# Kernel optimization log

Hardware: AMD Instinct MI355X
Metric: run time of the kernel (lower is better)

The kernel has to match this reference:

```python
import jax, jax.numpy as jnp
import numpy as np

N_CLASSES = 80
N_ANCHORS = 3
IMAGE_SIZE = 608
STRIDE = 8
FSIZE = IMAGE_SIZE // STRIDE  # 76
BATCH = 16
N_BOX = 100
N_CH = 5 + N_CLASSES
IGNORE_THRE = 0.5
ANCHORS_PX = np.array([[13, 16], [28, 32], [62, 35]], dtype=np.float32)
MASKED_ANCHORS = ANCHORS_PX / IMAGE_SIZE / STRIDE  # grid-normalized anchors, [3,2]


def _bce(x, t):
    # torch F.binary_cross_entropy with log terms clamped at -100
    return -(t * jnp.maximum(jnp.log(x), -100.0)
             + (1.0 - t) * jnp.maximum(jnp.log(1.0 - x), -100.0))


def _iou_xyxy_ciou(a, b):
    # a: [N,4] xyxy, b: [M,4] xyxy -> CIoU [N,M] (standard YOLOv4 bboxes_iou, CIoU=True)
    tl = jnp.maximum(a[:, None, :2], b[None, :, :2])
    br = jnp.minimum(a[:, None, 2:], b[None, :, 2:])
    con_tl = jnp.minimum(a[:, None, :2], b[None, :, :2])
    con_br = jnp.maximum(a[:, None, 2:], b[None, :, 2:])
    area_a = jnp.prod(a[:, 2:] - a[:, :2], -1)
    area_b = jnp.prod(b[:, 2:] - b[:, :2], -1)
    en = jnp.all(tl < br, -1).astype(a.dtype)
    area_i = jnp.prod(br - tl, -1) * en
    iou = area_i / jnp.maximum(area_a[:, None] + area_b[None, :] - area_i, 1e-16)
    ctr_a = (a[:, :2] + a[:, 2:]) * 0.5
    ctr_b = (b[:, :2] + b[:, 2:]) * 0.5
    wh_a = a[:, 2:] - a[:, :2]
    wh_b = b[:, 2:] - b[:, :2]
    rho2 = jnp.sum((ctr_a[:, None] - ctr_b[None, :]) ** 2, -1)
    c2 = jnp.sum((con_br - con_tl) ** 2, -1)
    v = (4.0 / np.pi ** 2) * (jnp.arctan(wh_a[:, None, 0] / jnp.maximum(wh_a[:, None, 1], 1e-16))
                              - jnp.arctan(wh_b[None, :, 0] / jnp.maximum(wh_b[None, :, 1], 1e-16))) ** 2
    alpha = v / jnp.maximum(1.0 - iou + v, 1e-16)
    return iou - rho2 / jnp.maximum(c2, 1e-16) - alpha * v


def _iou_cxcywh(a, b):
    # a: [N,4] cx,cy,w,h ; b: [M,4] -> plain IoU [N,M]
    tl = jnp.maximum(a[:, None, :2] - a[:, None, 2:] * 0.5, b[None, :, :2] - b[None, :, 2:] * 0.5)
    br = jnp.minimum(a[:, None, :2] + a[:, None, 2:] * 0.5, b[None, :, :2] + b[None, :, 2:] * 0.5)
    area_a = jnp.prod(a[:, 2:], -1)
    area_b = jnp.prod(b[:, 2:], -1)
    en = jnp.all(tl < br, -1).astype(a.dtype)
    area_i = jnp.prod(br - tl, -1) * en
    return area_i / jnp.maximum(area_a[:, None] + area_b[None, :] - area_i, 1e-16)


def _prepare_one(pred_b, labels_b, masked_anchors, ref_anchors):
    # pred_b: [A,f,f,4] (cx,cy,w,h in grid units); labels_b: [N,5]
    n = labels_b.shape[0]
    lx = (labels_b[:, 0] + labels_b[:, 2]) / (STRIDE * 2)
    ly = (labels_b[:, 1] + labels_b[:, 3]) / (STRIDE * 2)
    lw = labels_b[:, 2] / STRIDE
    lh = labels_b[:, 3] / STRIDE
    li = lx.astype(jnp.int32)  # trunc toward zero (values positive)
    lj = ly.astype(jnp.int32)
    # anchor matching on (0,0,w,h) corner boxes vs ref anchors, CIoU
    box_wh = jnp.stack([jnp.zeros_like(lw), jnp.zeros_like(lh), lw, lh], -1)
    best_n_all = jnp.argmax(_iou_xyxy_ciou(box_wh, ref_anchors), axis=1)
    best_n = best_n_all % N_ANCHORS
    valid = best_n_all < N_ANCHORS  # anchor_masks == [0,1,2] -> always True here
    # ignore mask from pred IoU vs full label boxes
    label_box = jnp.stack([lx, ly, lw, lh], -1)
    pred_ious = _iou_cxcywh(pred_b.reshape(-1, 4), label_box)  # [A*f*f, N]
    obj = (~(jnp.max(pred_ious, axis=1) > IGNORE_THRE)).astype(jnp.float32)  # flat
    ncell = N_ANCHORS * FSIZE * FSIZE
    flat = jnp.where(valid, best_n * FSIZE * FSIZE + lj * FSIZE + li, ncell)  # OOB -> dropped
    obj = obj.at[flat].set(1.0, mode='drop')
    tmask = jnp.zeros((ncell, 4 + N_CLASSES), jnp.float32).at[flat].set(1.0, mode='drop')
    tx = lx - jnp.trunc(lx)
    aw = masked_anchors[best_n, 0]
    ah = masked_anchors[best_n, 1]
    rows = jnp.zeros((n, N_CH), jnp.float32)
    rows = rows.at[:, 0].set(tx).at[:, 1].set(tx)  # original uses label_x for both (kept faithful)
    rows = rows.at[:, 2].set(jnp.log(lw / aw + 1e-16))
    rows = rows.at[:, 3].set(jnp.log(lh / ah + 1e-16))
    rows = rows.at[:, 4].set(1.0)
    cls = labels_b[:, 4].astype(jnp.int32)
    rows = rows.at[jnp.arange(n), 5 + cls].set(1.0)
    target = jnp.zeros((ncell, N_CH), jnp.float32).at[flat].set(rows, mode='drop')
    scale_v = jnp.sqrt(2.0 - lw * lh / (FSIZE * FSIZE))
    tscale = jnp.zeros((ncell, 2), jnp.float32).at[flat].set(
        jnp.stack([scale_v, scale_v], -1), mode='drop')
    shp = (N_ANCHORS, FSIZE, FSIZE)
    return (obj.reshape(shp), tmask.reshape(shp + (4 + N_CLASSES,)),
            tscale.reshape(shp + (2,)), target.reshape(shp + (N_CH,)))


def _forward(x, labels):
    B = x.shape[0]
    out = x.reshape(B, N_ANCHORS, N_CH, FSIZE, FSIZE).transpose(0, 1, 3, 4, 2)
    sig = jax.nn.sigmoid(out)
    o01 = sig[..., :2]     # sigmoided xy
    o23r = out[..., 2:4]   # raw wh
    o4 = sig[..., 4]       # sigmoided obj
    ocls = sig[..., 5:]    # sigmoided cls
    grid = jnp.arange(FSIZE, dtype=x.dtype)
    masked_anchors = jnp.asarray(MASKED_ANCHORS)
    aw = masked_anchors[:, 0][None, :, None, None]
    ah = masked_anchors[:, 1][None, :, None, None]
    px = o01[..., 0] + grid[None, None, None, :]
    py = o01[..., 1] + grid[None, None, :, None]
    pw = jnp.exp(o23r[..., 0] * aw)  # faithful to original exp(raw * anchor)
    ph = jnp.exp(o23r[..., 1] * ah)
    pred_bbox = jnp.stack([px, py, pw, ph], -1)  # [B,3,f,f,4]
    ref_anchors = jnp.zeros((N_ANCHORS, 4), jnp.float32).at[:, 2:].set(masked_anchors)
    obj_mask, target_mask, target_scale, target = jax.vmap(
        _prepare_one, in_axes=(0, 0, None, None))(pred_bbox, labels, masked_anchors, ref_anchors)
    m01 = target_mask[..., :2]
    m23 = target_mask[..., 2:4]
    mcls = target_mask[..., 4:]
    o01m = o01 * m01
    o23m = o23r * m23 * target_scale
    o4m = o4 * obj_mask
    oclsm = ocls * mcls
    t01 = target[..., :2] * m01
    t23 = target[..., 2:4] * m23 * target_scale
    t4 = target[..., 4] * obj_mask
    tcls = target[..., 5:] * mcls
    w = target_scale * target_scale
    loss_xy = jnp.sum(w * _bce(o01m, t01))
    loss_wh = jnp.sum((o23m - t23) ** 2) / 2
    loss_obj = jnp.sum(_bce(o4m, t4))
    loss_cls = jnp.sum(_bce(oclsm, tcls))
    out_full = jnp.concatenate([o01m, o23m, o4m[..., None], oclsm], -1)
    tgt_full = jnp.concatenate([t01, t23, t4[..., None], tcls], -1)
    loss_l2 = jnp.sum((out_full - tgt_full) ** 2)
    loss = loss_xy + loss_wh + loss_obj + loss_cls
    return loss, loss_xy, loss_wh, loss_obj, loss_cls, loss_l2


def setup_inputs() -> dict:
    key = jax.random.key(0)
    k1, k2, k3, k4 = jax.random.split(key, 4)
    x = jax.random.normal(k1, (BATCH, N_ANCHORS * N_CH, FSIZE, FSIZE), jnp.float32)
    xy = jax.random.uniform(k2, (BATCH, N_BOX, 2), jnp.float32, 0.0, IMAGE_SIZE / 2)
    wh = jax.random.uniform(k3, (BATCH, N_BOX, 2), jnp.float32, float(STRIDE), IMAGE_SIZE / 2)
    cls = jax.random.randint(k4, (BATCH, N_BOX, 1), 0, N_CLASSES).astype(jnp.float32)
    labels = jnp.concatenate([xy, wh, cls], -1)  # [B, N_BOX, 5]
    return {"x": x, "labels": labels}


def reference(x, labels):
    return _forward(x, labels)
```

## Files before the change

kernel.cpp:

```cpp
#include <hip/hip_runtime.h>
#include <math.h>

#define FS      76
#define NCELLP  (FS*FS)
#define NA      3
#define NCH     85
#define NB      16
#define NLAB    100
#define NCLS    80
#define BLK     256
#define GX      ((NCELLP + BLK - 1) / BLK)
#define NBLK    (GX * NA * NB)

__device__ __forceinline__ float sigf(float z) { return 1.0f / (1.0f + expf(-z)); }

__device__ __forceinline__ float bcef(float x, float t) {
    return -(t * fmaxf(logf(x), -100.0f) + (1.0f - t) * fmaxf(logf(1.0f - x), -100.0f));
}

__global__ __launch_bounds__(BLK) void k_main(const float* __restrict__ x,
                                              const float* __restrict__ labels,
                                              double* __restrict__ part)
{
    const float AW[3] = {13.0f/4864.0f, 28.0f/4864.0f, 62.0f/4864.0f};
    const float AH[3] = {16.0f/4864.0f, 32.0f/4864.0f, 35.0f/4864.0f};

    __shared__ float4 s_box[NLAB];
    __shared__ float  s_area[NLAB];
    __shared__ int    s_flat[NLAB];
    __shared__ float  s_tx[NLAB], s_tw[NLAB], s_th[NLAB], s_sv[NLAB];
    __shared__ int    s_cls[NLAB];
    __shared__ int    s_win[BLK];
    __shared__ float4 s_cbox[NLAB];
    __shared__ float  s_carea[NLAB];
    __shared__ int    s_ncand, s_nw;
    __shared__ int    s_wlist[BLK];
    __shared__ float  s_pmax[BLK/64];
    __shared__ float  s_red[BLK/64][5];

    const int a = blockIdx.y, b = blockIdx.z;
    const int tid = threadIdx.x;

    s_win[tid] = -1;
    if (tid == 0) { s_ncand = 0; s_nw = 0; }
    if (tid < NLAB) {
        const float* L = labels + (size_t)(b * NLAB + tid) * 5;
        const float lx = (L[0] + L[2]) * 0.0625f;
        const float ly = (L[1] + L[3]) * 0.0625f;
        const float lw = L[2] * 0.125f;
        const float lh = L[3] * 0.125f;
        const int li = (int)lx, lj = (int)ly;

        const float area_a = lw * lh;
        const float ata = atanf(lw / fmaxf(lh, 1e-16f));
        const float V4PI2 = (float)(4.0 / (M_PI * M_PI));
        float best = -1e30f; int bn = 0;
        #pragma unroll
        for (int n = 0; n < NA; n++) {
            const float aw = AW[n], ah = AH[n];
            const float brx = fminf(lw, aw), bry = fminf(lh, ah);
            const float ai  = (0.0f < brx && 0.0f < bry) ? brx * bry : 0.0f;
            const float iou = ai / fmaxf(area_a + aw * ah - ai, 1e-16f);
            const float dx = (lw - aw) * 0.5f, dy = (lh - ah) * 0.5f;
            const float rho2 = dx * dx + dy * dy;
            const float cx = fmaxf(lw, aw), cy = fmaxf(lh, ah);
            const float c2 = cx * cx + cy * cy;
            const float da = ata - atanf(aw / fmaxf(ah, 1e-16f));
            const float v = V4PI2 * da * da;
            const float alpha = v / fmaxf(1.0f - iou + v, 1e-16f);
            const float ciou = iou - rho2 / fmaxf(c2, 1e-16f) - alpha * v;
            if (ciou > best) { best = ciou; bn = n; }
        }
        s_box[tid]  = make_float4(lx - lw * 0.5f, ly - lh * 0.5f,
                                  lx + lw * 0.5f, ly + lh * 0.5f);
        s_area[tid] = area_a;
        s_flat[tid] = bn * NCELLP + lj * FS + li;
        s_tx[tid]   = lx - truncf(lx);
        s_tw[tid]   = logf(lw / AW[bn] + 1e-16f);
        s_th[tid]   = logf(lh / AH[bn] + 1e-16f);
        s_sv[tid]   = sqrtf(2.0f - area_a / (float)NCELLP);
        s_cls[tid]  = (int)L[4];
    }
    __syncthreads();

    const int p = blockIdx.x * BLK + tid;
    const bool live = (p < NCELLP);
    const int pc = live ? p : (NCELLP - 1);
    const float* xb = x + ((size_t)(b * NA + a) * NCH) * NCELLP + pc;
    const float o0 = xb[0];
    const float o1 = xb[(size_t)1 * NCELLP];
    const float o2 = xb[(size_t)2 * NCELLP];
    const float o3 = xb[(size_t)3 * NCELLP];
    const float o4 = xb[(size_t)4 * NCELLP];
    const float s0 = sigf(o0), s1 = sigf(o1), s4 = sigf(o4);
    const float pw = expf(o2 * AW[a]), ph = expf(o3 * AH[a]);
    const float pa = live ? pw * ph : 0.0f;

    if (tid < NLAB) {
        const int idx = s_flat[tid] - (a * NCELLP + blockIdx.x * BLK);
        if (idx >= 0 && idx < BLK) atomicMax(&s_win[idx], tid);
    }
    float m = pa;
    #pragma unroll
    for (int off = 32; off > 0; off >>= 1) m = fmaxf(m, __shfl_xor(m, off, 64));
    if ((tid & 63) == 0) s_pmax[tid >> 6] = m;
    __syncthreads();
    const float pmax = fmaxf(fmaxf(s_pmax[0], s_pmax[1]), fmaxf(s_pmax[2], s_pmax[3]));

    if (tid < NLAB && s_area[tid] < 2.0f * pmax) {
        const int q = atomicAdd(&s_ncand, 1);
        s_cbox[q] = s_box[tid];
        s_carea[q] = s_area[tid];
    }
    __syncthreads();

    float axy = 0.f, awh = 0.f, aobj = 0.f, acls = 0.f, al2 = 0.f;
    int win = -1;
    if (live) {
        const int j = p / FS, i = p - j * FS;
        const float px = s0 + (float)i, py = s1 + (float)j;
        const float px1 = px - pw * 0.5f, px2 = px + pw * 0.5f;
        const float py1 = py - ph * 0.5f, py2 = py + ph * 0.5f;

        bool anyhit = false;
        const int nc = s_ncand;
        for (int l = 0; l < nc; l++) {
            const float4 bb = s_cbox[l];
            const float tlx = fmaxf(px1, bb.x);
            const float tly = fmaxf(py1, bb.y);
            const float brx = fminf(px2, bb.z);
            const float bry = fminf(py2, bb.w);
            const float ai = (tlx < brx && tly < bry) ? (brx - tlx) * (bry - tly) : 0.0f;
            anyhit = anyhit || (2.0f * ai > pa + s_carea[l] - ai);
        }
        win = s_win[tid];

        const float obj = (win >= 0) ? 1.0f : (anyhit ? 0.0f : 1.0f);
        if (obj != 0.0f) {
            const float t4 = (win >= 0) ? 1.0f : 0.0f;
            aobj += bcef(s4, t4);
            const float d4 = s4 - t4;
            al2 += d4 * d4;
        }
        if (win >= 0) {
            const float tx = s_tx[win], tw = s_tw[win], th = s_th[win], sv = s_sv[win];
            const float w2 = sv * sv;
            axy += w2 * (bcef(s0, tx) + bcef(s1, tx));
            const float dw = (o2 - tw) * sv, dh = (o3 - th) * sv;
            awh += dw * dw + dh * dh;
            const float d0 = s0 - tx, d1 = s1 - tx;
            al2 += d0 * d0 + d1 * d1 + dw * dw + dh * dh;
            const int q = atomicAdd(&s_nw, 1);
            s_wlist[q] = (tid << 16) | win;
        }
    }
    __syncthreads();

    const int nw = s_nw;
    for (int e = 0; e < nw; e++) {
        const int pk = s_wlist[e];
        const int wtid = pk >> 16, wl = pk & 0xffff;
        if (tid < NCLS) {
            const int cellp = blockIdx.x * BLK + wtid;
            const float sc = sigf(x[((size_t)(b * NA + a) * NCH + 5 + tid) * NCELLP + cellp]);
            const float t = (tid == s_cls[wl]) ? 1.0f : 0.0f;
            acls += bcef(sc, t);
            const float dc = sc - t;
            al2 += dc * dc;
        }
    }

    float v[5] = {axy, awh, aobj, acls, al2};
    #pragma unroll
    for (int k = 0; k < 5; k++) {
        float t = v[k];
        for (int off = 32; off > 0; off >>= 1) t += __shfl_down(t, off, 64);
        v[k] = t;
    }
    const int wave = tid >> 6, lane = tid & 63;
    if (lane == 0) {
        #pragma unroll
        for (int k = 0; k < 5; k++) s_red[wave][k] = v[k];
    }
    __syncthreads();
    if (tid == 0) {
        const int bid = blockIdx.x + GX * (blockIdx.y + NA * blockIdx.z);
        #pragma unroll
        for (int k = 0; k < 5; k++) {
            double s = 0.0;
            for (int w = 0; w < BLK/64; w++) s += (double)s_red[w][k];
            part[(size_t)bid * 5 + k] = s;
        }
    }
}

__global__ __launch_bounds__(256) void k_final(const double* __restrict__ part,
                                               float* __restrict__ out)
{
    __shared__ double s_red[4][5];
    const int tid = threadIdx.x;
    double v[5] = {0, 0, 0, 0, 0};
    for (int r = tid; r < NBLK; r += 256) {
        #pragma unroll
        for (int k = 0; k < 5; k++) v[k] += part[(size_t)r * 5 + k];
    }
    #pragma unroll
    for (int k = 0; k < 5; k++) {
        double t = v[k];
        for (int off = 32; off > 0; off >>= 1) t += __shfl_down(t, off, 64);
        v[k] = t;
    }
    const int wave = tid >> 6, lane = tid & 63;
    if (lane == 0) {
        #pragma unroll
        for (int k = 0; k < 5; k++) s_red[wave][k] = v[k];
    }
    __syncthreads();
    if (tid == 0) {
        double xy = 0, wh = 0, ob = 0, cl = 0, l2 = 0;
        for (int w = 0; w < 4; w++) {
            xy += s_red[w][0]; wh += s_red[w][1]; ob += s_red[w][2];
            cl += s_red[w][3]; l2 += s_red[w][4];
        }
        wh *= 0.5;
        out[0] = (float)(xy + wh + ob + cl);
        out[1] = (float)xy;
        out[2] = (float)wh;
        out[3] = (float)ob;
        out[4] = (float)cl;
        out[5] = (float)l2;
    }
}

extern "C" void kernel_launch(void* const* d_in, const int* in_sizes, int n_in,
                              void* d_out, int out_size, void* d_ws, size_t ws_size,
                              hipStream_t stream) {
    const float* x      = (const float*)d_in[0];
    const float* labels = (const float*)d_in[1];
    double* part = (double*)d_ws;

    dim3 grid(GX, NA, NB);
    k_main<<<grid, BLK, 0, stream>>>(x, labels, part);
    k_final<<<1, 256, 0, stream>>>(part, (float*)d_out);
}
```

Before: 132.4 us.

## Fuse final reduction via float atomics and hoist global loads before label setup

Drops the second reduction kernel: each block now adds its partial sums straight into the six outputs with float atomicAdd, after a memset of the output. The five channel loads from x are moved ahead of the label preprocessing so their latency overlaps the per-label CIoU and atan math. The per-wave pmax exchange is replaced by an integer atomicMax on the float bits, which is valid because the values are non-negative. The output now accumulates in float with a nondeterministic order instead of a double tree, and a memset is added to the launch sequence.

```diff
diff --git a/kernel.cpp b/kernel.cpp
--- a/kernel.cpp
+++ b/kernel.cpp
@@ -10,7 +10,6 @@
 #define NCLS    80
 #define BLK     256
 #define GX      ((NCELLP + BLK - 1) / BLK)
-#define NBLK    (GX * NA * NB)
 
 __device__ __forceinline__ float sigf(float z) { return 1.0f / (1.0f + expf(-z)); }
 
@@ -20,7 +19,7 @@
 
 __global__ __launch_bounds__(BLK) void k_main(const float* __restrict__ x,
                                               const float* __restrict__ labels,
-                                              double* __restrict__ part)
+                                              float* __restrict__ out)
 {
     const float AW[3] = {13.0f/4864.0f, 28.0f/4864.0f, 62.0f/4864.0f};
     const float AH[3] = {16.0f/4864.0f, 32.0f/4864.0f, 35.0f/4864.0f};
@@ -33,16 +32,25 @@
     __shared__ int    s_win[BLK];
     __shared__ float4 s_cbox[NLAB];
     __shared__ float  s_carea[NLAB];
-    __shared__ int    s_ncand, s_nw;
+    __shared__ int    s_ncand, s_nw, s_pmaxbits;
     __shared__ int    s_wlist[BLK];
-    __shared__ float  s_pmax[BLK/64];
     __shared__ float  s_red[BLK/64][5];
 
     const int a = blockIdx.y, b = blockIdx.z;
     const int tid = threadIdx.x;
 
+    const int p = blockIdx.x * BLK + tid;
+    const bool live = (p < NCELLP);
+    const int pc = live ? p : (NCELLP - 1);
+    const float* xb = x + ((size_t)(b * NA + a) * NCH) * NCELLP + pc;
+    const float o0 = xb[0];
+    const float o1 = xb[(size_t)1 * NCELLP];
+    const float o2 = xb[(size_t)2 * NCELLP];
+    const float o3 = xb[(size_t)3 * NCELLP];
+    const float o4 = xb[(size_t)4 * NCELLP];
+
     s_win[tid] = -1;
-    if (tid == 0) { s_ncand = 0; s_nw = 0; }
+    if (tid == 0) { s_ncand = 0; s_nw = 0; s_pmaxbits = 0; }
     if (tid < NLAB) {
         const float* L = labels + (size_t)(b * NLAB + tid) * 5;
         const float lx = (L[0] + L[2]) * 0.0625f;
@@ -83,15 +91,6 @@
     }
     __syncthreads();
 
-    const int p = blockIdx.x * BLK + tid;
-    const bool live = (p < NCELLP);
-    const int pc = live ? p : (NCELLP - 1);
-    const float* xb = x + ((size_t)(b * NA + a) * NCH) * NCELLP + pc;
-    const float o0 = xb[0];
-    const float o1 = xb[(size_t)1 * NCELLP];
-    const float o2 = xb[(size_t)2 * NCELLP];
-    const float o3 = xb[(size_t)3 * NCELLP];
-    const float o4 = xb[(size_t)4 * NCELLP];
     const float s0 = sigf(o0), s1 = sigf(o1), s4 = sigf(o4);
     const float pw = expf(o2 * AW[a]), ph = expf(o3 * AH[a]);
     const float pa = live ? pw * ph : 0.0f;
@@ -103,9 +102,9 @@
     float m = pa;
     #pragma unroll
     for (int off = 32; off > 0; off >>= 1) m = fmaxf(m, __shfl_xor(m, off, 64));
-    if ((tid & 63) == 0) s_pmax[tid >> 6] = m;
-    __syncthreads();
-    const float pmax = fmaxf(fmaxf(s_pmax[0], s_pmax[1]), fmaxf(s_pmax[2], s_pmax[3]));
+    if ((tid & 63) == 0) atomicMax(&s_pmaxbits, __float_as_int(m));
+    __syncthreads();
+    const float pmax = __int_as_float(s_pmaxbits);
 
     if (tid < NLAB && s_area[tid] < 2.0f * pmax) {
         const int q = atomicAdd(&s_ncand, 1);
@@ -115,7 +114,6 @@
     __syncthreads();
 
     float axy = 0.f, awh = 0.f, aobj = 0.f, acls = 0.f, al2 = 0.f;
-    int win = -1;
     if (live) {
         const int j = p / FS, i = p - j * FS;
         const float px = s0 + (float)i, py = s1 + (float)j;
@@ -133,7 +131,7 @@
             const float ai = (tlx < brx && tly < bry) ? (brx - tlx) * (bry - tly) : 0.0f;
             anyhit = anyhit || (2.0f * ai > pa + s_carea[l] - ai);
         }
-        win = s_win[tid];
+        const int win = s_win[tid];
 
         const float obj = (win >= 0) ? 1.0f : (anyhit ? 0.0f : 1.0f);
         if (obj != 0.0f) {
@@ -184,51 +182,22 @@
     }
     __syncthreads();
     if (tid == 0) {
-        const int bid = blockIdx.x + GX * (blockIdx.y + NA * blockIdx.z);
+        double s[5];
         #pragma unroll
         for (int k = 0; k < 5; k++) {
-            double s = 0.0;
-            for (int w = 0; w < BLK/64; w++) s += (double)s_red[w][k];
-            part[(size_t)bid * 5 + k] = s;
-        }
-    }
-}
-
-__global__ __launch_bounds__(256) void k_final(const double* __restrict__ part,
-                                               float* __restrict__ out)
-{
-    __shared__ double s_red[4][5];
-    const int tid = threadIdx.x;
-    double v[5] = {0, 0, 0, 0, 0};
-    for (int r = tid; r < NBLK; r += 256) {
-        #pragma unroll
-        for (int k = 0; k < 5; k++) v[k] += part[(size_t)r * 5 + k];
-    }
-    #pragma unroll
-    for (int k = 0; k < 5; k++) {
-        double t = v[k];
-        for (int off = 32; off > 0; off >>= 1) t += __shfl_down(t, off, 64);
-        v[k] = t;
-    }
-    const int wave = tid >> 6, lane = tid & 63;
-    if (lane == 0) {
-        #pragma unroll
-        for (int k = 0; k < 5; k++) s_red[wave][k] = v[k];
-    }
-    __syncthreads();
-    if (tid == 0) {
-        double xy = 0, wh = 0, ob = 0, cl = 0, l2 = 0;
-        for (int w = 0; w < 4; w++) {
-            xy += s_red[w][0]; wh += s_red[w][1]; ob += s_red[w][2];
-            cl += s_red[w][3]; l2 += s_red[w][4];
-        }
-        wh *= 0.5;
-        out[0] = (float)(xy + wh + ob + cl);
-        out[1] = (float)xy;
-        out[2] = (float)wh;
-        out[3] = (float)ob;
-        out[4] = (float)cl;
-        out[5] = (float)l2;
+            double t = 0.0;
+            for (int w = 0; w < BLK/64; w++) t += (double)s_red[w][k];
+            s[k] = t;
+        }
+        s[1] *= 0.5;
+        const float xy = (float)s[0], wh = (float)s[1], ob = (float)s[2],
+                    cl = (float)s[3], l2 = (float)s[4];
+        atomicAdd(&out[0], xy + wh + ob + cl);
+        atomicAdd(&out[1], xy);
+        atomicAdd(&out[2], wh);
+        atomicAdd(&out[3], ob);
+        atomicAdd(&out[4], cl);
+        atomicAdd(&out[5], l2);
     }
 }
 
@@ -237,9 +206,10 @@
                               hipStream_t stream) {
     const float* x      = (const float*)d_in[0];
     const float* labels = (const float*)d_in[1];
-    double* part = (double*)d_ws;
+    float* out = (float*)d_out;
+
+    hipMemsetAsync(out, 0, 6 * sizeof(float), stream);
 
     dim3 grid(GX, NA, NB);
-    k_main<<<grid, BLK, 0, stream>>>(x, labels, part);
-    k_final<<<1, 256, 0, stream>>>(part, (float*)d_out);
+    k_main<<<grid, BLK, 0, stream>>>(x, labels, out);
 }
```

Result: slower. 208.5 us (+57.5%).

## Fuse final reduction into main kernel via last-block counter and hoist loads

Applied to the files above, without the earlier changes.

Removes the separate k_final launch: each block writes its partial sums, bumps a global atomic counter, and the last block to finish does the final reduction and writes the outputs. Loads of the five prediction channels are moved before the label-prep section so their latency overlaps that work. The per-wave max is now combined with a shared atomicMax on float bits instead of a small array. A hipMemsetAsync is added each call to reset the counter, so one extra stream operation replaces the kernel launch.

```diff
diff --git a/kernel.cpp b/kernel.cpp
--- a/kernel.cpp
+++ b/kernel.cpp
@@ -20,7 +20,9 @@
 
 __global__ __launch_bounds__(BLK) void k_main(const float* __restrict__ x,
                                               const float* __restrict__ labels,
-                                              double* __restrict__ part)
+                                              double* __restrict__ part,
+                                              unsigned int* __restrict__ counter,
+                                              float* __restrict__ out)
 {
     const float AW[3] = {13.0f/4864.0f, 28.0f/4864.0f, 62.0f/4864.0f};
     const float AH[3] = {16.0f/4864.0f, 32.0f/4864.0f, 35.0f/4864.0f};
@@ -33,16 +35,26 @@
     __shared__ int    s_win[BLK];
     __shared__ float4 s_cbox[NLAB];
     __shared__ float  s_carea[NLAB];
-    __shared__ int    s_ncand, s_nw;
+    __shared__ int    s_ncand, s_nw, s_pmaxbits, s_last;
     __shared__ int    s_wlist[BLK];
-    __shared__ float  s_pmax[BLK/64];
     __shared__ float  s_red[BLK/64][5];
+    __shared__ double s_dred[BLK/64][5];
 
     const int a = blockIdx.y, b = blockIdx.z;
     const int tid = threadIdx.x;
 
+    const int p = blockIdx.x * BLK + tid;
+    const bool live = (p < NCELLP);
+    const int pc = live ? p : (NCELLP - 1);
+    const float* xb = x + ((size_t)(b * NA + a) * NCH) * NCELLP + pc;
+    const float o0 = xb[0];
+    const float o1 = xb[(size_t)1 * NCELLP];
+    const float o2 = xb[(size_t)2 * NCELLP];
+    const float o3 = xb[(size_t)3 * NCELLP];
+    const float o4 = xb[(size_t)4 * NCELLP];
+
     s_win[tid] = -1;
-    if (tid == 0) { s_ncand = 0; s_nw = 0; }
+    if (tid == 0) { s_ncand = 0; s_nw = 0; s_pmaxbits = 0; }
     if (tid < NLAB) {
         const float* L = labels + (size_t)(b * NLAB + tid) * 5;
         const float lx = (L[0] + L[2]) * 0.0625f;
@@ -83,15 +95,6 @@
     }
     __syncthreads();
 
-    const int p = blockIdx.x * BLK + tid;
-    const bool live = (p < NCELLP);
-    const int pc = live ? p : (NCELLP - 1);
-    const float* xb = x + ((size_t)(b * NA + a) * NCH) * NCELLP + pc;
-    const float o0 = xb[0];
-    const float o1 = xb[(size_t)1 * NCELLP];
-    const float o2 = xb[(size_t)2 * NCELLP];
-    const float o3 = xb[(size_t)3 * NCELLP];
-    const float o4 = xb[(size_t)4 * NCELLP];
     const float s0 = sigf(o0), s1 = sigf(o1), s4 = sigf(o4);
     const float pw = expf(o2 * AW[a]), ph = expf(o3 * AH[a]);
     const float pa = live ? pw * ph : 0.0f;
@@ -103,9 +106,9 @@
     float m = pa;
     #pragma unroll
     for (int off = 32; off > 0; off >>= 1) m = fmaxf(m, __shfl_xor(m, off, 64));
-    if ((tid & 63) == 0) s_pmax[tid >> 6] = m;
-    __syncthreads();
-    const float pmax = fmaxf(fmaxf(s_pmax[0], s_pmax[1]), fmaxf(s_pmax[2], s_pmax[3]));
+    if ((tid & 63) == 0) atomicMax(&s_pmaxbits, __float_as_int(m));
+    __syncthreads();
+    const float pmax = __int_as_float(s_pmaxbits);
 
     if (tid < NLAB && s_area[tid] < 2.0f * pmax) {
         const int q = atomicAdd(&s_ncand, 1);
@@ -115,7 +118,6 @@
     __syncthreads();
 
     float axy = 0.f, awh = 0.f, aobj = 0.f, acls = 0.f, al2 = 0.f;
-    int win = -1;
     if (live) {
         const int j = p / FS, i = p - j * FS;
         const float px = s0 + (float)i, py = s1 + (float)j;
@@ -133,7 +135,7 @@
             const float ai = (tlx < brx && tly < bry) ? (brx - tlx) * (bry - tly) : 0.0f;
             anyhit = anyhit || (2.0f * ai > pa + s_carea[l] - ai);
         }
-        win = s_win[tid];
+        const int win = s_win[tid];
 
         const float obj = (win >= 0) ? 1.0f : (anyhit ? 0.0f : 1.0f);
         if (obj != 0.0f) {
@@ -183,52 +185,53 @@
         for (int k = 0; k < 5; k++) s_red[wave][k] = v[k];
     }
     __syncthreads();
+
+    const int bid = blockIdx.x + GX * (blockIdx.y + NA * blockIdx.z);
     if (tid == 0) {
-        const int bid = blockIdx.x + GX * (blockIdx.y + NA * blockIdx.z);
         #pragma unroll
         for (int k = 0; k < 5; k++) {
-            double s = 0.0;
-            for (int w = 0; w < BLK/64; w++) s += (double)s_red[w][k];
-            part[(size_t)bid * 5 + k] = s;
-        }
-    }
-}
-
-__global__ __launch_bounds__(256) void k_final(const double* __restrict__ part,
-                                               float* __restrict__ out)
-{
-    __shared__ double s_red[4][5];
-    const int tid = threadIdx.x;
-    double v[5] = {0, 0, 0, 0, 0};
-    for (int r = tid; r < NBLK; r += 256) {
-        #pragma unroll
-        for (int k = 0; k < 5; k++) v[k] += part[(size_t)r * 5 + k];
-    }
-    #pragma unroll
-    for (int k = 0; k < 5; k++) {
-        double t = v[k];
-        for (int off = 32; off > 0; off >>= 1) t += __shfl_down(t, off, 64);
-        v[k] = t;
-    }
-    const int wave = tid >> 6, lane = tid & 63;
-    if (lane == 0) {
-        #pragma unroll
-        for (int k = 0; k < 5; k++) s_red[wave][k] = v[k];
-    }
-    __syncthreads();
-    if (tid == 0) {
-        double xy = 0, wh = 0, ob = 0, cl = 0, l2 = 0;
-        for (int w = 0; w < 4; w++) {
-            xy += s_red[w][0]; wh += s_red[w][1]; ob += s_red[w][2];
-            cl += s_red[w][3]; l2 += s_red[w][4];
-        }
-        wh *= 0.5;
-        out[0] = (float)(xy + wh + ob + cl);
-        out[1] = (float)xy;
-        out[2] = (float)wh;
-        out[3] = (float)ob;
-        out[4] = (float)cl;
-        out[5] = (float)l2;
+            double t = 0.0;
+            for (int w = 0; w < BLK/64; w++) t += (double)s_red[w][k];
+            part[(size_t)bid * 5 + k] = t;
+        }
+        __threadfence();
+        const unsigned int old = atomicAdd(counter, 1u);
+        s_last = (old == NBLK - 1) ? 1 : 0;
+    }
+    __syncthreads();
+
+    if (s_last) {
+        __threadfence();
+        double u[5] = {0, 0, 0, 0, 0};
+        for (int r = tid; r < NBLK; r += BLK) {
+            #pragma unroll
+            for (int k = 0; k < 5; k++) u[k] += part[(size_t)r * 5 + k];
+        }
+        #pragma unroll
+        for (int k = 0; k < 5; k++) {
+            double t = u[k];
+            for (int off = 32; off > 0; off >>= 1) t += __shfl_down(t, off, 64);
+            u[k] = t;
+        }
+        if (lane == 0) {
+            #pragma unroll
+            for (int k = 0; k < 5; k++) s_dred[wave][k] = u[k];
+        }
+        __syncthreads();
+        if (tid == 0) {
+            double xy = 0, wh = 0, ob = 0, cl = 0, l2 = 0;
+            for (int w = 0; w < BLK/64; w++) {
+                xy += s_dred[w][0]; wh += s_dred[w][1]; ob += s_dred[w][2];
+                cl += s_dred[w][3]; l2 += s_dred[w][4];
+            }
+            wh *= 0.5;
+            out[0] = (float)(xy + wh + ob + cl);
+            out[1] = (float)xy;
+            out[2] = (float)wh;
+            out[3] = (float)ob;
+            out[4] = (float)cl;
+            out[5] = (float)l2;
+        }
     }
 }
 
@@ -238,8 +241,10 @@
     const float* x      = (const float*)d_in[0];
     const float* labels = (const float*)d_in[1];
     double* part = (double*)d_ws;
+    unsigned int* counter = (unsigned int*)((char*)d_ws + (size_t)NBLK * 5 * sizeof(double));
+
+    hipMemsetAsync(counter, 0, sizeof(unsigned int), stream);
 
     dim3 grid(GX, NA, NB);
-    k_main<<<grid, BLK, 0, stream>>>(x, labels, part);
-    k_final<<<1, 256, 0, stream>>>(part, (float*)d_out);
+    k_main<<<grid, BLK, 0, stream>>>(x, labels, part, counter, (float*)d_out);
 }
```

New measurement: 176.0 us. +33.0%, slower.
